# Performance work log

Hardware: AMD Instinct MI355X
Metric: run time of the kernel (lower is better)

The kernel has to match this reference:

```python
import jax, jax.numpy as jnp
import numpy as np

B, IN_CH, OUT_CH, T, N_STATE, FACTOR = 8, 128, 128, 16384, 256, 2
DT = 1.0
LN_EPS = 1e-5


def setup_inputs() -> dict:
    key = jax.random.key(0)
    k = jax.random.split(key, 5)
    x = jax.random.normal(k[0], (B, IN_CH, T), jnp.float32)
    raw_lambda = jnp.zeros((N_STATE,), jnp.float32)
    B_c = jax.random.normal(k[1], (IN_CH, N_STATE), jnp.float32) * (1.0 / np.sqrt(IN_CH))
    C_mat = jax.random.normal(k[2], (N_STATE, OUT_CH), jnp.float32) * (1.0 / np.sqrt(N_STATE))
    ln_gamma = jnp.ones((OUT_CH,), jnp.float32)
    ln_beta = jnp.zeros((OUT_CH,), jnp.float32)
    # Conv1d(out_ch*factor, out_ch, kernel_size=1): weight (out, in), bias (out,)
    W = jax.random.normal(k[3], (OUT_CH, OUT_CH * FACTOR), jnp.float32) * (1.0 / np.sqrt(OUT_CH * FACTOR))
    b = jax.random.normal(k[4], (OUT_CH,), jnp.float32) * 0.01
    return {"x": x, "raw_lambda": raw_lambda, "B_c": B_c, "C_mat": C_mat,
            "ln_gamma": ln_gamma, "ln_beta": ln_beta, "W": W, "b": b}


def reference(x, raw_lambda, B_c, C_mat, ln_gamma, ln_beta, W, b):
    # --- SSMLayerZOH ---
    lam = -jax.nn.softplus(raw_lambda)              # (N,) continuous diag, < 0
    A_d = jnp.exp(lam * DT)                         # ZOH discretized diag
    B_d = B_c * ((A_d - 1.0) / lam)[None, :]        # (IN, N)
    v = jnp.einsum('bct,cn->tbn', x, B_d)           # per-step input injection

    def step(s, vt):
        s = s * A_d + vt
        return s, s

    s0 = jnp.zeros((x.shape[0], lam.shape[0]), x.dtype)
    _, ss = jax.lax.scan(step, s0, v)               # (T, B, N)
    y = jnp.einsum('tbn,no->bto', ss, C_mat)        # (B, T, OUT)

    # --- LayerNorm(out_ch) + SiLU ---
    mu = jnp.mean(y, axis=-1, keepdims=True)
    var = jnp.mean((y - mu) ** 2, axis=-1, keepdims=True)
    h = (y - mu) / jnp.sqrt(var + LN_EPS) * ln_gamma + ln_beta
    h = h * jax.nn.sigmoid(h)                       # SiLU

    # --- Resample (factor > 1 branch): downsample T, stack factor into channels ---
    h = jnp.transpose(h, (0, 2, 1))                 # (B, OUT, T)
    Bn, C, Tt = h.shape
    hr = h.reshape(Bn, C, Tt // FACTOR, FACTOR)
    hr = jnp.transpose(hr, (0, 1, 3, 2)).reshape(Bn, C * FACTOR, Tt // FACTOR)
    out = jnp.einsum('bct,oc->bot', hr, W) + b[None, :, None]  # conv1x1
    return out
```

## Files before the change

kernel.cpp:

```cpp
#include <hip/hip_runtime.h>

#define BATCH 8
#define CIN 128
#define OCH 128
#define T_LEN 16384
#define NS 256
#define CHUNK 64
#define NCHUNK (T_LEN / CHUNK)
#define THALF (T_LEN / 2)
#define SCHUNK 8192
#define SROW 260
#define HROW 132
#define NCHK 4

typedef __attribute__((ext_vector_type(8))) short bf16x8;
typedef __attribute__((ext_vector_type(4))) float f32x4;
typedef __attribute__((ext_vector_type(4))) unsigned int u32x4;

__device__ __forceinline__ unsigned int pk2(float lo, float hi) {
  unsigned int d;
  asm("v_cvt_pk_bf16_f32 %0, %1, %2" : "=v"(d) : "v"(lo), "v"(hi));
  return d;
}
__device__ __forceinline__ unsigned short f2bf(float f) {
  unsigned int u = __float_as_uint(f);
  u += 0x7fffu + ((u >> 16) & 1u);
  return (unsigned short)(u >> 16);
}
__device__ __forceinline__ float softplusf_(float v) {
  return (v > 20.0f) ? v : log1pf(expf(v));
}
__device__ __forceinline__ void rawbar() {
  __builtin_amdgcn_sched_barrier(0);
  asm volatile("s_waitcnt lgkmcnt(0)" ::: "memory");
  __builtin_amdgcn_sched_barrier(0);
  __builtin_amdgcn_s_barrier();
  __builtin_amdgcn_sched_barrier(0);
}

__global__ __launch_bounds__(256) void k_prep(
    const float* __restrict__ rl, const float* __restrict__ Bc,
    const float* __restrict__ Cm, const float* __restrict__ W,
    unsigned short* __restrict__ BdT, unsigned short* __restrict__ CT,
    unsigned short* __restrict__ Wb, float* __restrict__ Ad, float* __restrict__ rL,
    float* __restrict__ PWf)
{
  const int tid = blockIdx.x * 256 + threadIdx.x;
  if (tid < NS * CIN) {
    const int n = tid >> 7, c = tid & 127;
    float lam = -softplusf_(rl[n]);
    float ad = expf(lam);
    float sc = (ad - 1.0f) / lam;
    BdT[tid] = f2bf(Bc[c * NS + n] * sc);
  } else if (tid < 2 * NS * CIN) {
    const int i = tid - NS * CIN;
    const int o = i >> 8, n = i & 255;
    CT[i] = f2bf(Cm[n * OCH + o]);
  } else if (tid < 3 * NS * CIN) {
    const int i = tid - 2 * NS * CIN;
    Wb[i] = f2bf(W[i]);
  } else if (tid < 3 * NS * CIN + NS) {
    const int n = tid - 3 * NS * CIN;
    float lam = -softplusf_(rl[n]);
    Ad[n] = expf(lam);
    rL[n] = expf(lam * (float)CHUNK);
  } else if (tid < 3 * NS * CIN + NS + 32 * NS) {
    const int i = tid - (3 * NS * CIN + NS);
    const int tp = i >> 8, n = i & 255;
    float lam = -softplusf_(rl[n]);
    PWf[i] = expf(lam * (float)(2 * tp + 1));
  }
}

__global__ __launch_bounds__(256) void k_combine(float* __restrict__ carry,
                                                 const float* __restrict__ rL)
{
  const int b = blockIdx.x >> 3;
  const int ng = blockIdx.x & 7;
  const int t = threadIdx.x;
  __shared__ float Y[32][NCHUNK];
  float* base = carry + ((size_t)b * NCHUNK + t) * NS + ng * 32;
  #pragma unroll
  for (int i4 = 0; i4 < 8; ++i4) {
    float4 q = *(const float4*)(base + i4 * 4);
    Y[i4 * 4 + 0][t] = q.x; Y[i4 * 4 + 1][t] = q.y;
    Y[i4 * 4 + 2][t] = q.z; Y[i4 * 4 + 3][t] = q.w;
  }
  float rp[32];
  #pragma unroll
  for (int i = 0; i < 32; ++i) rp[i] = rL[ng * 32 + i];
  __syncthreads();
  for (int d = 1; d < NCHUNK; d <<= 1) {
    float tmp[32];
    #pragma unroll
    for (int i = 0; i < 32; ++i) tmp[i] = (t >= d) ? Y[i][t - d] : 0.0f;
    __syncthreads();
    #pragma unroll
    for (int i = 0; i < 32; ++i) { Y[i][t] += rp[i] * tmp[i]; rp[i] *= rp[i]; }
    __syncthreads();
  }
  const int tm = (t == 0) ? 0 : (t - 1);
  #pragma unroll
  for (int i4 = 0; i4 < 8; ++i4) {
    float a = Y[i4 * 4 + 0][tm], bb = Y[i4 * 4 + 1][tm];
    float c = Y[i4 * 4 + 2][tm], dd = Y[i4 * 4 + 3][tm];
    float4 q;
    q.x = (t == 0) ? 0.0f : a;  q.y = (t == 0) ? 0.0f : bb;
    q.z = (t == 0) ? 0.0f : c;  q.w = (t == 0) ? 0.0f : dd;
    *(float4*)(base + i4 * 4) = q;
  }
}

__global__ __launch_bounds__(512, 4) void k_scan(
    const float* __restrict__ x,
    const unsigned short* __restrict__ BdT,
    const float* __restrict__ Ad,
    unsigned int* __restrict__ s0,
    float* __restrict__ carry)
{
  const int bid = blockIdx.x;
  const int b = bid >> 8;
  const int kc = bid & 255;
  const int tid = threadIdx.x;
  const int w = tid >> 6, l = tid & 63, l15 = l & 15, g = l >> 4;

  __shared__ __align__(16) unsigned int Xt[64 * 64];

  {
    const int c2 = w * 8 + (l & 7);
    const int t0b = (l >> 3) * 8;
    const float* r0 = x + ((size_t)(b * CIN + 2 * c2)) * T_LEN + kc * CHUNK + t0b;
    const f32x4 xa0 = *(const f32x4*)r0;
    const f32x4 xa1 = *(const f32x4*)(r0 + 4);
    const f32x4 xb0 = *(const f32x4*)(r0 + T_LEN);
    const f32x4 xb1 = *(const f32x4*)(r0 + T_LEN + 4);
    #pragma unroll
    for (int k = 0; k < 8; ++k) {
      const int t = t0b + k;
      const float va = (k < 4) ? xa0[k & 3] : xa1[k & 3];
      const float vb = (k < 4) ? xb0[k & 3] : xb1[k & 3];
      Xt[t * 64 + (c2 ^ ((t & 7) << 2))] = pk2(va, vb);
    }
  }

  bf16x8 Bf[2][4];
  #pragma unroll
  for (int nt = 0; nt < 2; ++nt)
    #pragma unroll
    for (int kt = 0; kt < 4; ++kt)
      Bf[nt][kt] = *(const bf16x8*)&BdT[(w * 32 + nt * 16 + l15) * CIN + kt * 32 + g * 8];

  float A1[2], A2[2], A3[2], A4[2], A8[2], A16[2], A4G[2], M1[2], M2[2];
  #pragma unroll
  for (int nt = 0; nt < 2; ++nt) {
    const float a1 = Ad[w * 32 + nt * 16 + l15];
    A1[nt] = a1; A2[nt] = a1 * a1; A3[nt] = A2[nt] * a1; A4[nt] = A2[nt] * A2[nt];
    A8[nt] = A4[nt] * A4[nt]; A16[nt] = A8[nt] * A8[nt];
    float a4g = 1.0f;
    if (g & 1) a4g *= A4[nt];
    if (g & 2) a4g *= A8[nt];
    A4G[nt] = a4g;
    M1[nt] = (g >= 1) ? A4[nt] : 0.0f;
    M2[nt] = (g >= 2) ? A8[nt] : 0.0f;
  }
  __syncthreads();

  f32x4 vac[4][2] = {};
  #pragma unroll
  for (int kt = 0; kt < 4; ++kt) {
    bf16x8 afr[4];
    #pragma unroll
    for (int mt = 0; mt < 4; ++mt)
      afr[mt] = *(const bf16x8*)&Xt[(mt * 16 + l15) * 64 + ((kt * 16 + g * 4) ^ ((l15 & 7) << 2))];
    #pragma unroll
    for (int nt = 0; nt < 2; ++nt)
      #pragma unroll
      for (int mt = 0; mt < 4; ++mt)
        vac[mt][nt] = __builtin_amdgcn_mfma_f32_16x16x32_bf16(afr[mt], Bf[nt][kt], vac[mt][nt], 0, 0, 0);
  }

  float crv[2];
  #pragma unroll
  for (int nt = 0; nt < 2; ++nt) {
    float cr = 0.0f;
    #pragma unroll
    for (int mt = 0; mt < 4; ++mt) {
      const float p0 = vac[mt][nt][0];
      const float p1 = fmaf(A1[nt], p0, vac[mt][nt][1]);
      const float p2 = fmaf(A1[nt], p1, vac[mt][nt][2]);
      const float p3 = fmaf(A1[nt], p2, vac[mt][nt][3]);
      float c0 = p3;
      float u = __shfl_up(c0, 16);
      c0 = fmaf(M1[nt], u, c0);
      u = __shfl_up(c0, 32);
      c0 = fmaf(M2[nt], u, c0);
      float e = __shfl_up(c0, 16);
      e = (g == 0) ? 0.0f : e;
      const float seed = fmaf(A4G[nt], cr, e);
      vac[mt][nt][0] = fmaf(A1[nt], seed, p0);
      vac[mt][nt][1] = fmaf(A2[nt], seed, p1);
      vac[mt][nt][2] = fmaf(A3[nt], seed, p2);
      vac[mt][nt][3] = fmaf(A4[nt], seed, p3);
      const float ctop = __shfl(c0, 48 + l15);
      cr = fmaf(A16[nt], cr, ctop);
    }
    crv[nt] = cr;
  }

  unsigned int* sc = s0 + (size_t)(b * NCHUNK + kc) * SCHUNK;
  #pragma unroll
  for (int mt = 0; mt < 4; ++mt)
    #pragma unroll
    for (int nt = 0; nt < 2; ++nt) {
      const int n = w * 32 + nt * 16 + l15;
      #pragma unroll
      for (int rp = 0; rp < 2; ++rp) {
        const int tp = mt * 8 + g * 2 + rp;
        sc[tp * 256 + n] = pk2(vac[mt][nt][rp * 2], vac[mt][nt][rp * 2 + 1]);
      }
    }
  if (g == 0) {
    #pragma unroll
    for (int nt = 0; nt < 2; ++nt)
      carry[((size_t)b * NCHUNK + kc) * NS + (w * 32 + nt * 16 + l15)] = crv[nt];
  }
}

__global__ __launch_bounds__(512, 2) void k_apply(
    const unsigned int* __restrict__ S,
    const unsigned short* __restrict__ CT,
    const unsigned short* __restrict__ Wb,
    const float* __restrict__ PWf,
    const float* __restrict__ Ad,
    const float* __restrict__ carry,
    const float* __restrict__ lng, const float* __restrict__ lnb,
    const float* __restrict__ bias,
    float* __restrict__ out)
{
  const int bid = blockIdx.x;
  const int b = bid / (NCHUNK / NCHK);
  const int kc0 = (bid % (NCHUNK / NCHK)) * NCHK;
  const int tid = threadIdx.x;
  const int w = tid >> 6, l = tid & 63, l15 = l & 15, g = l >> 4;
  const int tt = w >> 2, oq = w & 3;

  __shared__ __align__(16) unsigned int V2[2][32 * SROW];
  __shared__ __align__(16) float Lexf[64 * 8];

  const unsigned int sel = (l15 & 1) ? 0x07060302u : 0x05040100u;
  const f32x4 adv = *(const f32x4*)&Ad[4 * l];

  bf16x8 ctf[8][2];
  #pragma unroll
  for (int kt = 0; kt < 8; ++kt)
    #pragma unroll
    for (int ot = 0; ot < 2; ++ot)
      ctf[kt][ot] = *(const bf16x8*)&CT[(oq * 32 + ot * 16 + l15) * NS + kt * 32 + g * 8];
  bf16x8 wf[8];
  #pragma unroll
  for (int kt = 0; kt < 8; ++kt)
    wf[kt] = *(const bf16x8*)&Wb[(w * 16 + l15) * NS + kt * 32 + g * 8];
  const float ga0 = lng[oq * 32 + l15],      be0 = lnb[oq * 32 + l15];
  const float ga1 = lng[oq * 32 + 16 + l15], be1 = lnb[oq * 32 + 16 + l15];
  const float bia = bias[w * 16 + l15];

  u32x4 st0, st1, st2, st3;
  f32x4 sd;

#define LOAD_ST(KC) do {                                                    \
    const unsigned int* scb_ = S + (size_t)(b * NCHUNK + (KC)) * SCHUNK;    \
    st0 = *(const u32x4*)&scb_[0 * 2048 + tid * 4];                         \
    st1 = *(const u32x4*)&scb_[1 * 2048 + tid * 4];                         \
    st2 = *(const u32x4*)&scb_[2 * 2048 + tid * 4];                         \
    st3 = *(const u32x4*)&scb_[3 * 2048 + tid * 4];                         \
    sd  = *(const f32x4*)&carry[((size_t)b * NCHUNK + (KC)) * NS + 4 * l];  \
  } while (0)

#define CORRECT_ROW(QV, RR) do {                                            \
    const f32x4 pw_ = *(const f32x4*)&PWf[((RR) * 8 + w) * 256 + 4 * l];    \
    const float e00 = sd[0] * pw_[0];                                       \
    const float e01 = sd[1] * pw_[1];                                       \
    const float e02 = sd[2] * pw_[2];                                       \
    const float e03 = sd[3] * pw_[3];                                       \
    QV[0] = pk2(__uint_as_float(QV[0] << 16) + e00,                         \
                __uint_as_float(QV[0] & 0xffff0000u) + e00 * adv[0]);       \
    QV[1] = pk2(__uint_as_float(QV[1] << 16) + e01,                         \
                __uint_as_float(QV[1] & 0xffff0000u) + e01 * adv[1]);       \
    QV[2] = pk2(__uint_as_float(QV[2] << 16) + e02,                         \
                __uint_as_float(QV[2] & 0xffff0000u) + e02 * adv[2]);       \
    QV[3] = pk2(__uint_as_float(QV[3] << 16) + e03,                         \
                __uint_as_float(QV[3] & 0xffff0000u) + e03 * adv[3]);       \
    *(u32x4*)&dst_[((RR) * 8 + w) * SROW + 4 * l] = QV;                     \
  } while (0)

#define CORRECT_STORE(DST) do {                                             \
    unsigned int* dst_ = (DST);                                             \
    CORRECT_ROW(st0, 0);                                                    \
    CORRECT_ROW(st1, 1);                                                    \
    CORRECT_ROW(st2, 2);                                                    \
    CORRECT_ROW(st3, 3);                                                    \
  } while (0)

  LOAD_ST(kc0);
  CORRECT_STORE(&V2[0][0]);
  LOAD_ST(kc0 + 1);
  rawbar();

  #pragma unroll 1
  for (int i = 0; i < NCHK; ++i) {
    const int cur = i & 1;
    const int kc = kc0 + i;

    f32x4 yac[2][2] = {};
    #pragma unroll
    for (int kt = 0; kt < 8; ++kt) {
      const int n0 = kt * 32 + g * 8;
      bf16x8 As[2];
      #pragma unroll
      for (int mt = 0; mt < 2; ++mt) {
        const int tp = (tt * 32 + mt * 16 + l15) >> 1;
        const u32x4 q0 = *(const u32x4*)&V2[cur][tp * SROW + n0];
        const u32x4 q1 = *(const u32x4*)&V2[cur][tp * SROW + n0 + 4];
        union { bf16x8 v; unsigned int u[4]; } Aa;
        Aa.u[0] = __builtin_amdgcn_perm(q0[1], q0[0], sel);
        Aa.u[1] = __builtin_amdgcn_perm(q0[3], q0[2], sel);
        Aa.u[2] = __builtin_amdgcn_perm(q1[1], q1[0], sel);
        Aa.u[3] = __builtin_amdgcn_perm(q1[3], q1[2], sel);
        As[mt] = Aa.v;
      }
      #pragma unroll
      for (int ot = 0; ot < 2; ++ot)
        #pragma unroll
        for (int mt = 0; mt < 2; ++mt)
          yac[mt][ot] = __builtin_amdgcn_mfma_f32_16x16x32_bf16(As[mt], ctf[kt][ot], yac[mt][ot], 0, 0, 0);
    }
    #pragma unroll
    for (int mt = 0; mt < 2; ++mt)
      #pragma unroll
      for (int r = 0; r < 4; ++r) {
        float s1 = yac[mt][0][r] + yac[mt][1][r];
        float s2 = yac[mt][0][r] * yac[mt][0][r] + yac[mt][1][r] * yac[mt][1][r];
        #pragma unroll
        for (int d = 1; d < 16; d <<= 1) { s1 += __shfl_xor(s1, d); s2 += __shfl_xor(s2, d); }
        if (l15 == 0) {
          const int t = tt * 32 + mt * 16 + g * 4 + r;
          *(float2*)&Lexf[t * 8 + oq * 2] = make_float2(s1, s2);
        }
      }
    rawbar();

    unsigned int* Hr = &V2[cur][0];
    #pragma unroll
    for (int mt = 0; mt < 2; ++mt) {
      float mu[4], rs[4];
      #pragma unroll
      for (int r = 0; r < 4; ++r) {
        const int t = tt * 32 + mt * 16 + g * 4 + r;
        const float4 f0 = *(const float4*)&Lexf[t * 8];
        const float4 f1 = *(const float4*)&Lexf[t * 8 + 4];
        const float m = (f0.x + f0.z + f1.x + f1.z) * (1.0f / 128.0f);
        const float va = (f0.y + f0.w + f1.y + f1.w) * (1.0f / 128.0f) - m * m;
        mu[r] = m;
        rs[r] = rsqrtf(va + 1e-5f);
      }
      #pragma unroll
      for (int ot = 0; ot < 2; ++ot) {
        const int o = oq * 32 + ot * 16 + l15;
        const float ga = ot ? ga1 : ga0;
        const float be = ot ? be1 : be0;
        #pragma unroll
        for (int rp = 0; rp < 2; ++rp) {
          float h0 = (yac[mt][ot][rp * 2] - mu[rp * 2]) * rs[rp * 2] * ga + be;
          h0 = h0 * __builtin_amdgcn_rcpf(1.0f + __expf(-h0));
          float h1 = (yac[mt][ot][rp * 2 + 1] - mu[rp * 2 + 1]) * rs[rp * 2 + 1] * ga + be;
          h1 = h1 * __builtin_amdgcn_rcpf(1.0f + __expf(-h1));
          const int t2 = tt * 16 + mt * 8 + g * 2 + rp;
          Hr[t2 * HROW + o] = pk2(h0, h1);
        }
      }
    }
    if (i + 1 < NCHK) {
      CORRECT_STORE(&V2[cur ^ 1][0]);
      if (i + 2 < NCHK) LOAD_ST(kc + 2);
    }
    rawbar();

    {
      f32x4 oac[2] = {};
      #pragma unroll
      for (int kt = 0; kt < 8; ++kt) {
        bf16x8 Aa0, Aa1;
        {
          union { bf16x8 v; u32x4 u; } Ax;
          Ax.u = *(const u32x4*)&Hr[(l15) * HROW + kt * 16 + g * 4];
          Aa0 = Ax.v;
          Ax.u = *(const u32x4*)&Hr[(16 + l15) * HROW + kt * 16 + g * 4];
          Aa1 = Ax.v;
        }
        oac[0] = __builtin_amdgcn_mfma_f32_16x16x32_bf16(Aa0, wf[kt], oac[0], 0, 0, 0);
        oac[1] = __builtin_amdgcn_mfma_f32_16x16x32_bf16(Aa1, wf[kt], oac[1], 0, 0, 0);
      }
      const int o = w * 16 + l15;
      #pragma unroll
      for (int mt = 0; mt < 2; ++mt) {
        float4 q;
        q.x = oac[mt][0] + bia;
        q.y = oac[mt][1] + bia;
        q.z = oac[mt][2] + bia;
        q.w = oac[mt][3] + bia;
        *(float4*)(out + ((size_t)(b * OCH + o)) * THALF + kc * 32 + mt * 16 + g * 4) = q;
      }
    }
  }
#undef LOAD_ST
#undef CORRECT_ROW
#undef CORRECT_STORE
}

extern "C" void kernel_launch(void* const* d_in, const int* in_sizes, int n_in,
                              void* d_out, int out_size, void* d_ws, size_t ws_size,
                              hipStream_t stream) {
  const float* x    = (const float*)d_in[0];
  const float* rl   = (const float*)d_in[1];
  const float* Bc   = (const float*)d_in[2];
  const float* Cm   = (const float*)d_in[3];
  const float* lng  = (const float*)d_in[4];
  const float* lnb  = (const float*)d_in[5];
  const float* W    = (const float*)d_in[6];
  const float* bias = (const float*)d_in[7];
  float* out = (float*)d_out;

  char* ws = (char*)d_ws;
  unsigned short* BdT = (unsigned short*)(ws);
  unsigned short* CT  = (unsigned short*)(ws + 65536);
  unsigned short* Wb  = (unsigned short*)(ws + 131072);
  float* Ad    = (float*)(ws + 196608);
  float* rL    = (float*)(ws + 197632);
  float* PWf   = (float*)(ws + 198656);
  float* carry = (float*)(ws + 231424);
  unsigned int* S = (unsigned int*)(ws + 231424 + 2097152);

  k_prep<<<417, 256, 0, stream>>>(rl, Bc, Cm, W, BdT, CT, Wb, Ad, rL, PWf);
  k_scan<<<BATCH * NCHUNK, 512, 0, stream>>>(x, BdT, Ad, S, carry);
  k_combine<<<64, 256, 0, stream>>>(carry, rL);
  k_apply<<<BATCH * (NCHUNK / NCHK), 512, 0, stream>>>(S, CT, Wb, PWf, Ad, carry,
                                                       lng, lnb, bias, out);
}
```

Baseline: 104.5 us.

## Store corrected states de-interleaved with XOR-swizzled LDS layout, drop perm unpacking

```diff
diff --git a/kernel.cpp b/kernel.cpp
--- a/kernel.cpp
+++ b/kernel.cpp
@@ -9,7 +9,6 @@
 #define NCHUNK (T_LEN / CHUNK)
 #define THALF (T_LEN / 2)
 #define SCHUNK 8192
-#define SROW 260
 #define HROW 132
 #define NCHK 4
 
@@ -244,10 +243,9 @@
   const int w = tid >> 6, l = tid & 63, l15 = l & 15, g = l >> 4;
   const int tt = w >> 2, oq = w & 3;
 
-  __shared__ __align__(16) unsigned int V2[2][32 * SROW];
+  __shared__ __align__(16) unsigned short V2[2][64 * 256];
   __shared__ __align__(16) float Lexf[64 * 8];
 
-  const unsigned int sel = (l15 & 1) ? 0x07060302u : 0x05040100u;
   const f32x4 adv = *(const f32x4*)&Ad[4 * l];
 
   bf16x8 ctf[8][2];
@@ -260,6 +258,10 @@
   #pragma unroll
   for (int kt = 0; kt < 8; ++kt)
     wf[kt] = *(const bf16x8*)&Wb[(w * 16 + l15) * NS + kt * 32 + g * 8];
+  f32x4 pwv[4];
+  #pragma unroll
+  for (int r = 0; r < 4; ++r)
+    pwv[r] = *(const f32x4*)&PWf[(r * 8 + w) * 256 + 4 * l];
   const float ga0 = lng[oq * 32 + l15],      be0 = lnb[oq * 32 + l15];
   const float ga1 = lng[oq * 32 + 16 + l15], be1 = lnb[oq * 32 + 16 + l15];
   const float bia = bias[w * 16 + l15];
@@ -277,24 +279,28 @@
   } while (0)
 
 #define CORRECT_ROW(QV, RR) do {                                            \
-    const f32x4 pw_ = *(const f32x4*)&PWf[((RR) * 8 + w) * 256 + 4 * l];    \
-    const float e00 = sd[0] * pw_[0];                                       \
-    const float e01 = sd[1] * pw_[1];                                       \
-    const float e02 = sd[2] * pw_[2];                                       \
-    const float e03 = sd[3] * pw_[3];                                       \
-    QV[0] = pk2(__uint_as_float(QV[0] << 16) + e00,                         \
-                __uint_as_float(QV[0] & 0xffff0000u) + e00 * adv[0]);       \
-    QV[1] = pk2(__uint_as_float(QV[1] << 16) + e01,                         \
-                __uint_as_float(QV[1] & 0xffff0000u) + e01 * adv[1]);       \
-    QV[2] = pk2(__uint_as_float(QV[2] << 16) + e02,                         \
-                __uint_as_float(QV[2] & 0xffff0000u) + e02 * adv[2]);       \
-    QV[3] = pk2(__uint_as_float(QV[3] << 16) + e03,                         \
-                __uint_as_float(QV[3] & 0xffff0000u) + e03 * adv[3]);       \
-    *(u32x4*)&dst_[((RR) * 8 + w) * SROW + 4 * l] = QV;                     \
+    const float e00 = sd[0] * pwv[RR][0];                                   \
+    const float e01 = sd[1] * pwv[RR][1];                                   \
+    const float e02 = sd[2] * pwv[RR][2];                                   \
+    const float e03 = sd[3] * pwv[RR][3];                                   \
+    const float lo0 = __uint_as_float(QV[0] << 16) + e00;                   \
+    const float hi0 = __uint_as_float(QV[0] & 0xffff0000u) + e00 * adv[0];  \
+    const float lo1 = __uint_as_float(QV[1] << 16) + e01;                   \
+    const float hi1 = __uint_as_float(QV[1] & 0xffff0000u) + e01 * adv[1];  \
+    const float lo2 = __uint_as_float(QV[2] << 16) + e02;                   \
+    const float hi2 = __uint_as_float(QV[2] & 0xffff0000u) + e02 * adv[2];  \
+    const float lo3 = __uint_as_float(QV[3] << 16) + e03;                   \
+    const float hi3 = __uint_as_float(QV[3] & 0xffff0000u) + e03 * adv[3];  \
+    const int t0_ = ((RR) * 8 + w) * 2;                                     \
+    const int t1_ = t0_ + 1;                                                \
+    uint2 wlo; wlo.x = pk2(lo0, lo1); wlo.y = pk2(lo2, lo3);                \
+    uint2 whi; whi.x = pk2(hi0, hi1); whi.y = pk2(hi2, hi3);                \
+    *(uint2*)&dst_[t0_ * 256 + ((((l >> 1) ^ ((t0_ & 7) << 2)) << 3) | ((l & 1) << 2))] = wlo; \
+    *(uint2*)&dst_[t1_ * 256 + ((((l >> 1) ^ ((t1_ & 7) << 2)) << 3) | ((l & 1) << 2))] = whi; \
   } while (0)
 
 #define CORRECT_STORE(DST) do {                                             \
-    unsigned int* dst_ = (DST);                                             \
+    unsigned short* dst_ = (DST);                                           \
     CORRECT_ROW(st0, 0);                                                    \
     CORRECT_ROW(st1, 1);                                                    \
     CORRECT_ROW(st2, 2);                                                    \
@@ -314,19 +320,11 @@
     f32x4 yac[2][2] = {};
     #pragma unroll
     for (int kt = 0; kt < 8; ++kt) {
-      const int n0 = kt * 32 + g * 8;
       bf16x8 As[2];
       #pragma unroll
       for (int mt = 0; mt < 2; ++mt) {
-        const int tp = (tt * 32 + mt * 16 + l15) >> 1;
-        const u32x4 q0 = *(const u32x4*)&V2[cur][tp * SROW + n0];
-        const u32x4 q1 = *(const u32x4*)&V2[cur][tp * SROW + n0 + 4];
-        union { bf16x8 v; unsigned int u[4]; } Aa;
-        Aa.u[0] = __builtin_amdgcn_perm(q0[1], q0[0], sel);
-        Aa.u[1] = __builtin_amdgcn_perm(q0[3], q0[2], sel);
-        Aa.u[2] = __builtin_amdgcn_perm(q1[1], q1[0], sel);
-        Aa.u[3] = __builtin_amdgcn_perm(q1[3], q1[2], sel);
-        As[mt] = Aa.v;
+        const int t = tt * 32 + mt * 16 + l15;
+        As[mt] = *(const bf16x8*)&V2[cur][t * 256 + (((kt * 4 + g) ^ ((t & 7) << 2)) << 3)];
       }
       #pragma unroll
       for (int ot = 0; ot < 2; ++ot)
@@ -349,7 +347,7 @@
       }
     rawbar();
 
-    unsigned int* Hr = &V2[cur][0];
+    unsigned int* Hr = (unsigned int*)&V2[cur][0];
     #pragma unroll
     for (int mt = 0; mt < 2; ++mt) {
       float mu[4], rs[4];
```

After: 102.3 us. 2.1% less time.
